# Kernel tuning notes

Measured on AMD Instinct MI355X. Metric: run time of the kernel, lower is better.

## Reference

```python
import jax, jax.numpy as jnp
import numpy as np

N_NODES = 50000
N_REL = 16
N_BASIS = 8
D_IN = 64
D_HID = 64
N_CLASS = 16
N_EDGES = 800000


def setup_inputs() -> dict:
    key = jax.random.key(0)
    ks = jax.random.split(key, 9)
    x = jax.random.normal(ks[0], (N_NODES, D_IN), dtype=jnp.float32)
    edge_index = jax.random.randint(ks[1], (2, N_EDGES), 0, N_NODES, dtype=jnp.int64)
    edge_type = jax.random.randint(ks[2], (N_EDGES,), 0, N_REL, dtype=jnp.int64)
    s1 = 1.0 / np.sqrt(D_IN)
    s2 = 1.0 / np.sqrt(D_HID)
    # layer 1: basis decomposition W_r = sum_b coeffs[r,b] * bases[b]
    bases1 = jax.random.normal(ks[3], (N_BASIS, D_IN, D_HID), dtype=jnp.float32) * s1
    coeffs1 = jax.random.normal(ks[4], (N_REL, N_BASIS), dtype=jnp.float32)
    self1 = jax.random.normal(ks[5], (D_IN, D_HID), dtype=jnp.float32) * s1
    # layer 2
    bases2 = jax.random.normal(ks[6], (N_BASIS, D_HID, N_CLASS), dtype=jnp.float32) * s2
    coeffs2 = jax.random.normal(ks[7], (N_REL, N_BASIS), dtype=jnp.float32)
    self2 = jax.random.normal(ks[8], (D_HID, N_CLASS), dtype=jnp.float32) * s2
    return {"x": x, "bases1": bases1, "coeffs1": coeffs1, "self1": self1,
            "bases2": bases2, "coeffs2": coeffs2, "self2": self2,
            "edge_index": edge_index, "edge_type": edge_type}


def _rgcn_layer(h, bases, coeffs, self_w, src, seg_id, inv_c):
    # normalized messages gathered from source nodes: [E, d]
    msg = h[src] * inv_c[:, None]
    # fused per-(relation, target-node) segment reduce -> [R, N, d]
    agg = jax.ops.segment_sum(msg, seg_id, num_segments=N_REL * N_NODES)
    agg = agg.reshape(N_REL, N_NODES, -1)
    # per-relation weights from basis decomposition: [R, d_in, d_out]
    w_rel = jnp.einsum('rb,bio->rio', coeffs, bases)
    return jnp.einsum('rni,rio->no', agg, w_rel) + h @ self_w


def reference(x, bases1, coeffs1, self1, bases2, coeffs2, self2, edge_index, edge_type):
    src, dst = edge_index[0], edge_index[1]
    # normalization constants: per-relation in-degree of each target node
    counts = jnp.zeros((N_REL, N_NODES), dtype=jnp.float32).at[edge_type, dst].add(1.0)
    inv_c = 1.0 / jnp.maximum(counts[edge_type, dst], 1.0)  # [E]
    seg_id = edge_type * N_NODES + dst  # combined (relation, node) segment key
    h = jax.nn.relu(_rgcn_layer(x, bases1, coeffs1, self1, src, seg_id, inv_c))
    logits = _rgcn_layer(h, bases2, coeffs2, self2, src, seg_id, inv_c)
    return logits
```

## Files before the change

kernel.cpp:

```cpp
#include <hip/hip_runtime.h>

#define N_NODES 50000
#define N_REL 16
#define N_BASIS 8
#define N_EDGES 800000
#define G1_BLOCKS 782
#define SC_BLOCKS 3125
#define WREL_BLOCKS 340
#define ZERO_BLOCKS 49
#define CAP 64

typedef short s8v __attribute__((ext_vector_type(8)));
typedef float f4v __attribute__((ext_vector_type(4)));

__device__ inline unsigned short f2bf(float f) {
    union { float f; unsigned u; } v; v.f = f;
    unsigned r = (v.u + 0x7FFFu + ((v.u >> 16) & 1u)) >> 16;
    return (unsigned short)r;
}
__device__ inline float bf2f(unsigned short b) {
    union { unsigned u; float f; } v; v.u = ((unsigned)b) << 16;
    return v.f;
}
__device__ __forceinline__ void acc8(float* a, float inv, int4 p) {
    a[0] += inv * __int_as_float((int)((unsigned)p.x << 16));
    a[1] += inv * __int_as_float(p.x & (int)0xFFFF0000u);
    a[2] += inv * __int_as_float((int)((unsigned)p.y << 16));
    a[3] += inv * __int_as_float(p.y & (int)0xFFFF0000u);
    a[4] += inv * __int_as_float((int)((unsigned)p.z << 16));
    a[5] += inv * __int_as_float(p.z & (int)0xFFFF0000u);
    a[6] += inv * __int_as_float((int)((unsigned)p.w << 16));
    a[7] += inv * __int_as_float(p.w & (int)0xFFFF0000u);
}

__global__ __launch_bounds__(256) void k_pre(const float* __restrict__ b1, const float* __restrict__ c1,
                                             const float* __restrict__ s1f,
                                             const float* __restrict__ b2, const float* __restrict__ c2,
                                             const float* __restrict__ s2f,
                                             unsigned short* __restrict__ w1T,
                                             unsigned short* __restrict__ w2T,
                                             int* __restrict__ cursor) {
    int bid = blockIdx.x;
    if (bid >= WREL_BLOCKS) {
        int i = (bid - WREL_BLOCKS) * 256 + threadIdx.x;
        if (i < 12504) ((int4*)cursor)[i] = make_int4(0, 0, 0, 0);
        return;
    }
    int idx = bid * 256 + threadIdx.x;
    if (idx < 17 * 4096) {
        int r = idx >> 12, o = (idx >> 6) & 63, k = idx & 63;
        float acc = 0.f;
        if (r < 16) {
            #pragma unroll
            for (int b = 0; b < N_BASIS; b++) acc += c1[r * N_BASIS + b] * b1[b * 4096 + k * 64 + o];
        } else {
            acc = s1f[k * 64 + o];
        }
        w1T[idx] = f2bf(acc);
    } else {
        int idx2 = idx - 17 * 4096;
        if (idx2 < 17 * 1024) {
            int r = idx2 >> 10, o = (idx2 >> 6) & 15, k = idx2 & 63;
            float acc = 0.f;
            if (r < 16) {
                #pragma unroll
                for (int b = 0; b < N_BASIS; b++) acc += c2[r * N_BASIS + b] * b2[b * 1024 + k * 16 + o];
            } else {
                acc = s2f[k * 16 + o];
            }
            w2T[idx2] = f2bf(acc);
        }
    }
}

__device__ __forceinline__ void gemm1_tile(int tile, int tid,
                                           const float* __restrict__ x,
                                           const unsigned short* __restrict__ w1T,
                                           unsigned short* __restrict__ t1,
                                           unsigned short* __restrict__ h,
                                           unsigned short* wbuf,
                                           unsigned short* ou) {
    int wv = tid >> 6, lane = tid & 63;
    int m = lane & 15, q = lane >> 4;
    int nb = tile * 64 + wv * 16;
    bool active = (nb < N_NODES);
    int n = active ? (nb + m) : 0;

    const float* xr = x + (size_t)n * 64 + q * 8;
    float4 x0a = *(const float4*)(xr);
    float4 x0b = *(const float4*)(xr + 4);
    float4 x1a = *(const float4*)(xr + 32);
    float4 x1b = *(const float4*)(xr + 36);
    s8v b0, b1;
    b0[0] = f2bf(x0a.x); b0[1] = f2bf(x0a.y); b0[2] = f2bf(x0a.z); b0[3] = f2bf(x0a.w);
    b0[4] = f2bf(x0b.x); b0[5] = f2bf(x0b.y); b0[6] = f2bf(x0b.z); b0[7] = f2bf(x0b.w);
    b1[0] = f2bf(x1a.x); b1[1] = f2bf(x1a.y); b1[2] = f2bf(x1a.z); b1[3] = f2bf(x1a.w);
    b1[4] = f2bf(x1b.x); b1[5] = f2bf(x1b.y); b1[6] = f2bf(x1b.z); b1[7] = f2bf(x1b.w);

    int c0 = tid, c1 = tid + 256;
    int p0s = (c0 >> 3) * 64 + (((c0 & 7) ^ ((c0 >> 3) & 7)) << 3);
    int p1s = (c1 >> 3) * 64 + (((c1 & 7) ^ ((c1 >> 3) & 7)) << 3);

    {
        const int4* src = (const int4*)w1T;
        int4 v0 = src[c0], v1 = src[c1];
        *(int4*)&wbuf[p0s] = v0;
        *(int4*)&wbuf[p1s] = v1;
    }
    __syncthreads();

    for (int w = 0; w < 17; w++) {
        int cur = w & 1;
        if (w < 16) {
            const int4* src = (const int4*)w1T + (w + 1) * 512;
            int4 v0 = src[c0], v1 = src[c1];
            *(int4*)&wbuf[(cur ^ 1) * 4096 + p0s] = v0;
            *(int4*)&wbuf[(cur ^ 1) * 4096 + p1s] = v1;
        }
        #pragma unroll
        for (int ct = 0; ct < 4; ct++) {
            int ro = ct * 16 + m;
            int pa = q ^ (ro & 7);
            int pb = (4 + q) ^ (ro & 7);
            s8v A0 = *(const s8v*)&wbuf[cur * 4096 + ro * 64 + pa * 8];
            s8v A1 = *(const s8v*)&wbuf[cur * 4096 + ro * 64 + pb * 8];
            f4v acc = (f4v){0.f, 0.f, 0.f, 0.f};
            acc = __builtin_amdgcn_mfma_f32_16x16x32_bf16(A0, b0, acc, 0, 0, 0);
            acc = __builtin_amdgcn_mfma_f32_16x16x32_bf16(A1, b1, acc, 0, 0, 0);
            ushort4 o4;
            o4.x = f2bf(acc[0]); o4.y = f2bf(acc[1]); o4.z = f2bf(acc[2]); o4.w = f2bf(acc[3]);
            int g = ct * 2 + (q >> 1);
            int pg = g ^ (m & 7);
            *(ushort4*)&ou[wv * 1024 + m * 64 + pg * 8 + (q & 1) * 4] = o4;
        }
        if (active) {
            int r1 = lane >> 3, g1 = lane & 7;
            int pg1 = g1 ^ (r1 & 7);
            int4 d0 = *(const int4*)&ou[wv * 1024 + r1 * 64 + pg1 * 8];
            int4 d1 = *(const int4*)&ou[wv * 1024 + (r1 + 8) * 64 + pg1 * 8];
            unsigned short* base = (w < 16) ? (t1 + ((size_t)w * N_NODES + nb) * 64)
                                            : (h + (size_t)nb * 64);
            *(int4*)(base + lane * 8) = d0;
            *(int4*)(base + 512 + lane * 8) = d1;
        }
        __syncthreads();
    }
}

__global__ __launch_bounds__(256) void k_fused1(const float* __restrict__ x,
                                                const unsigned short* __restrict__ w1T,
                                                unsigned short* __restrict__ t1,
                                                unsigned short* __restrict__ h,
                                                const int* __restrict__ ei,
                                                const int* __restrict__ et,
                                                int* __restrict__ cursor,
                                                int* __restrict__ sed) {
    __shared__ __align__(16) unsigned short wbuf[2 * 4096];
    __shared__ __align__(16) unsigned short ou[4 * 1024];
    if (blockIdx.x >= G1_BLOCKS) {
        int e = (blockIdx.x - G1_BLOCKS) * 256 + threadIdx.x;
        if (e < N_EDGES) {
            int src = ei[e];
            int dst = ei[N_EDGES + e];
            int t = et[e];
            int pos = atomicAdd(&cursor[dst], 1);
            if (pos < CAP) sed[dst * CAP + pos] = (t << 16) | src;
        }
        return;
    }
    gemm1_tile(blockIdx.x, threadIdx.x, x, w1T, t1, h, wbuf, ou);
}

__global__ __launch_bounds__(256) void k_agg1(const int* __restrict__ cursor,
                                              const int* __restrict__ sed,
                                              const unsigned short* __restrict__ t1,
                                              unsigned short* __restrict__ h) {
    __shared__ int hist[4][16];
    int tid = threadIdx.x;
    int wv = tid >> 6, lane = tid & 63;
    int n = blockIdx.x * 4 + wv;
    int deg = cursor[n];
    deg = deg < CAP ? deg : CAP;
    const int* bucket = sed + n * CAP;

    if (lane < 16) hist[wv][lane] = 0;
    __syncthreads();
    if (lane < deg) {
        int en = bucket[lane];
        atomicAdd(&hist[wv][en >> 16], 1);
    }
    __syncthreads();

    int slot = lane >> 3;
    int d8 = lane & 7;
    float a[8];
    #pragma unroll
    for (int j = 0; j < 8; j++) a[j] = 0.f;
    for (int i = slot; i < deg; i += 16) {
        int e0 = bucket[i];
        bool has1 = (i + 8) < deg;
        int e1 = has1 ? bucket[i + 8] : e0;
        int t0 = e0 >> 16, s0 = e0 & 0xFFFF;
        int t1i = e1 >> 16, s1 = e1 & 0xFFFF;
        float inv0 = 1.0f / (float)hist[wv][t0];
        float inv1 = has1 ? (1.0f / (float)hist[wv][t1i]) : 0.f;
        int4 p0 = *(const int4*)(t1 + ((size_t)(t0 * N_NODES + s0)) * 64 + d8 * 8);
        int4 p1 = *(const int4*)(t1 + ((size_t)(t1i * N_NODES + s1)) * 64 + d8 * 8);
        acc8(a, inv0, p0);
        acc8(a, inv1, p1);
    }
    #pragma unroll
    for (int j = 0; j < 8; j++) {
        a[j] += __shfl_xor(a[j], 8, 64);
        a[j] += __shfl_xor(a[j], 16, 64);
        a[j] += __shfl_xor(a[j], 32, 64);
    }
    if (slot == 0) {
        size_t hi = (size_t)n * 64 + d8 * 8;
        int4 hv = *(const int4*)(h + hi);
        float b[8];
        b[0] = __int_as_float((int)((unsigned)hv.x << 16));
        b[1] = __int_as_float(hv.x & (int)0xFFFF0000u);
        b[2] = __int_as_float((int)((unsigned)hv.y << 16));
        b[3] = __int_as_float(hv.y & (int)0xFFFF0000u);
        b[4] = __int_as_float((int)((unsigned)hv.z << 16));
        b[5] = __int_as_float(hv.z & (int)0xFFFF0000u);
        b[6] = __int_as_float((int)((unsigned)hv.w << 16));
        b[7] = __int_as_float(hv.w & (int)0xFFFF0000u);
        ushort4 o0, o1;
        o0.x = f2bf(b[0] + a[0]); o0.y = f2bf(b[1] + a[1]);
        o0.z = f2bf(b[2] + a[2]); o0.w = f2bf(b[3] + a[3]);
        o1.x = f2bf(b[4] + a[4]); o1.y = f2bf(b[5] + a[5]);
        o1.z = f2bf(b[6] + a[6]); o1.w = f2bf(b[7] + a[7]);
        *(ushort4*)(h + hi) = o0;
        *(ushort4*)(h + hi + 4) = o1;
    }
}

__global__ __launch_bounds__(256) void k_gemm2(const unsigned short* __restrict__ h,
                                               const unsigned short* __restrict__ w2T,
                                               unsigned short* __restrict__ t2, float* __restrict__ out) {
    __shared__ __align__(16) unsigned short wall[272 * 64];
    int tid = threadIdx.x;
    int wv = tid >> 6, lane = tid & 63;
    int m = lane & 15, q = lane >> 4;
    int nb = blockIdx.x * 64 + wv * 16;

    for (int c = tid; c < 2176; c += 256) {
        int4 v = ((const int4*)w2T)[c];
        int row = c >> 3, g = c & 7;
        *(int4*)&wall[row * 64 + ((g ^ (row & 7)) << 3)] = v;
    }
    __syncthreads();
    if (nb >= N_NODES) return;
    int n = nb + m;

    s8v b0 = *(const s8v*)(h + (size_t)n * 64 + q * 8);
    s8v b1 = *(const s8v*)(h + (size_t)n * 64 + 32 + q * 8);
    #pragma unroll
    for (int j = 0; j < 8; j++) {
        if ((unsigned short)b0[j] & 0x8000u) b0[j] = 0;
        if ((unsigned short)b1[j] & 0x8000u) b1[j] = 0;
    }

    for (int w = 0; w < 17; w++) {
        int ro = w * 16 + m;
        int pa = q ^ (ro & 7);
        int pb = (4 + q) ^ (ro & 7);
        s8v A0 = *(const s8v*)&wall[ro * 64 + pa * 8];
        s8v A1 = *(const s8v*)&wall[ro * 64 + pb * 8];
        f4v acc = (f4v){0.f, 0.f, 0.f, 0.f};
        acc = __builtin_amdgcn_mfma_f32_16x16x32_bf16(A0, b0, acc, 0, 0, 0);
        acc = __builtin_amdgcn_mfma_f32_16x16x32_bf16(A1, b1, acc, 0, 0, 0);
        if (w < 16) {
            ushort4 o;
            o.x = f2bf(acc[0]); o.y = f2bf(acc[1]); o.z = f2bf(acc[2]); o.w = f2bf(acc[3]);
            *(ushort4*)(t2 + ((size_t)w * N_NODES + n) * 16 + q * 4) = o;
        } else {
            *(float4*)(out + (size_t)n * 16 + q * 4) = make_float4(acc[0], acc[1], acc[2], acc[3]);
        }
    }
}

__global__ __launch_bounds__(256) void k_agg2(const int* __restrict__ cursor,
                                              const int* __restrict__ sed,
                                              const unsigned short* __restrict__ t2,
                                              float* __restrict__ out) {
    __shared__ int hist[16][16];
    int tid = threadIdx.x;
    int j = tid >> 4;
    int sub = tid & 15;
    int n = blockIdx.x * 16 + j;
    int deg = cursor[n];
    deg = deg < CAP ? deg : CAP;
    const int* bucket = sed + n * CAP;

    hist[j][sub] = 0;
    __syncthreads();
    for (int i = sub; i < deg; i += 16) {
        int en = bucket[i];
        atomicAdd(&hist[j][en >> 16], 1);
    }
    __syncthreads();

    int slot = sub >> 1;
    int d2 = sub & 1;
    float a[8];
    #pragma unroll
    for (int k = 0; k < 8; k++) a[k] = 0.f;
    for (int i = slot; i < deg; i += 16) {
        int e0 = bucket[i];
        bool has1 = (i + 8) < deg;
        int e1 = has1 ? bucket[i + 8] : e0;
        int t0 = e0 >> 16, s0 = e0 & 0xFFFF;
        int t1i = e1 >> 16, s1 = e1 & 0xFFFF;
        float inv0 = 1.0f / (float)hist[j][t0];
        float inv1 = has1 ? (1.0f / (float)hist[j][t1i]) : 0.f;
        int4 p0 = *(const int4*)(t2 + ((size_t)(t0 * N_NODES + s0)) * 16 + d2 * 8);
        int4 p1 = *(const int4*)(t2 + ((size_t)(t1i * N_NODES + s1)) * 16 + d2 * 8);
        acc8(a, inv0, p0);
        acc8(a, inv1, p1);
    }
    #pragma unroll
    for (int k = 0; k < 8; k++) {
        a[k] += __shfl_xor(a[k], 2, 64);
        a[k] += __shfl_xor(a[k], 4, 64);
        a[k] += __shfl_xor(a[k], 8, 64);
    }
    if (slot == 0) {
        float* p = out + (size_t)n * 16 + d2 * 8;
        float4 c0 = *(const float4*)p;
        float4 c1 = *(const float4*)(p + 4);
        c0.x += a[0]; c0.y += a[1]; c0.z += a[2]; c0.w += a[3];
        c1.x += a[4]; c1.y += a[5]; c1.z += a[6]; c1.w += a[7];
        *(float4*)p = c0;
        *(float4*)(p + 4) = c1;
    }
}

extern "C" void kernel_launch(void* const* d_in, const int* in_sizes, int n_in,
                              void* d_out, int out_size, void* d_ws, size_t ws_size,
                              hipStream_t stream) {
    const float* x      = (const float*)d_in[0];
    const float* bases1 = (const float*)d_in[1];
    const float* coeffs1= (const float*)d_in[2];
    const float* self1  = (const float*)d_in[3];
    const float* bases2 = (const float*)d_in[4];
    const float* coeffs2= (const float*)d_in[5];
    const float* self2  = (const float*)d_in[6];
    const int*   ei     = (const int*)d_in[7];
    const int*   et     = (const int*)d_in[8];
    float* out = (float*)d_out;

    char* ws = (char*)d_ws;
    int*            cursor = (int*)(ws + 0);
    unsigned short* w1T    = (unsigned short*)(ws + 200064);
    unsigned short* w2T    = (unsigned short*)(ws + 339328);
    int*            sed    = (int*)(ws + 374144);
    unsigned short* h      = (unsigned short*)(ws + 13174144);
    unsigned short* t1     = (unsigned short*)(ws + 19574144);
    unsigned short* t2     = (unsigned short*)(ws + 121974144);

    k_pre<<<WREL_BLOCKS + ZERO_BLOCKS, 256, 0, stream>>>(
        bases1, coeffs1, self1, bases2, coeffs2, self2, w1T, w2T, cursor);
    k_fused1<<<G1_BLOCKS + SC_BLOCKS, 256, 0, stream>>>(x, w1T, t1, h, ei, et, cursor, sed);
    k_agg1<<<12500, 256, 0, stream>>>(cursor, sed, t1, h);
    k_gemm2<<<G1_BLOCKS, 256, 0, stream>>>(h, w2T, t2, out);
    k_agg2<<<SC_BLOCKS, 256, 0, stream>>>(cursor, sed, t2, out);
}
```

Before: 187.5 us.

## Partition edge bucketing into 8 sub-buckets to cut atomic contention

Edge scatter now splits each destination's cursor and bucket into 8 partitions chosen by block index (capacity 16 each), so concurrent atomics on the same node counter are spread out. The aggregation kernels first gather the partitions into a per-wave shared-memory list and then read edges from LDS. agg2 is remapped to one wave per node, with 4 lanes per 16-wide row and 16 edge slots per wave. The cost is an 8x larger cursor array to zero, more scattered bucket reads, and a risk of dropping edges if any partition sees more than 16 edges for one node.

```diff
diff --git a/kernel.cpp b/kernel.cpp
--- a/kernel.cpp
+++ b/kernel.cpp
@@ -7,8 +7,9 @@
 #define G1_BLOCKS 782
 #define SC_BLOCKS 3125
 #define WREL_BLOCKS 340
-#define ZERO_BLOCKS 49
-#define CAP 64
+#define ZERO_BLOCKS 391
+#define NPART 8
+#define CAPP 16
 
 typedef short s8v __attribute__((ext_vector_type(8)));
 typedef float f4v __attribute__((ext_vector_type(4)));
@@ -43,7 +44,7 @@
     int bid = blockIdx.x;
     if (bid >= WREL_BLOCKS) {
         int i = (bid - WREL_BLOCKS) * 256 + threadIdx.x;
-        if (i < 12504) ((int4*)cursor)[i] = make_int4(0, 0, 0, 0);
+        if (i < 100000) ((int4*)cursor)[i] = make_int4(0, 0, 0, 0);
         return;
     }
     int idx = bid * 256 + threadIdx.x;
@@ -159,37 +160,57 @@
     __shared__ __align__(16) unsigned short ou[4 * 1024];
     if (blockIdx.x >= G1_BLOCKS) {
         int e = (blockIdx.x - G1_BLOCKS) * 256 + threadIdx.x;
+        int p = blockIdx.x & 7;
         if (e < N_EDGES) {
             int src = ei[e];
             int dst = ei[N_EDGES + e];
             int t = et[e];
-            int pos = atomicAdd(&cursor[dst], 1);
-            if (pos < CAP) sed[dst * CAP + pos] = (t << 16) | src;
+            int pos = atomicAdd(&cursor[p * N_NODES + dst], 1);
+            if (pos < CAPP) sed[p * (N_NODES * CAPP) + dst * CAPP + pos] = (t << 16) | src;
         }
         return;
     }
     gemm1_tile(blockIdx.x, threadIdx.x, x, w1T, t1, h, wbuf, ou);
+}
+
+__device__ __forceinline__ int stage_node(int n, int lane,
+                                          const int* __restrict__ cursor,
+                                          const int* __restrict__ sed,
+                                          int* ent) {
+    int dp = 0;
+    if (lane < NPART) {
+        dp = cursor[lane * N_NODES + n];
+        dp = dp < CAPP ? dp : CAPP;
+    }
+    int p = lane >> 3, j = lane & 7;
+    int off = 0, deg = 0, mydeg = 0;
+    #pragma unroll
+    for (int q = 0; q < NPART; q++) {
+        int dq = __shfl(dp, q, 64);
+        if (q < p) off += dq;
+        if (q == p) mydeg = dq;
+        deg += dq;
+    }
+    const int* bucket = sed + p * (N_NODES * CAPP) + n * CAPP;
+    if (j < mydeg) ent[off + j] = bucket[j];
+    if (j + 8 < mydeg) ent[off + j + 8] = bucket[j + 8];
+    return deg;
 }
 
 __global__ __launch_bounds__(256) void k_agg1(const int* __restrict__ cursor,
                                               const int* __restrict__ sed,
                                               const unsigned short* __restrict__ t1,
                                               unsigned short* __restrict__ h) {
+    __shared__ int ent[4][128];
     __shared__ int hist[4][16];
     int tid = threadIdx.x;
     int wv = tid >> 6, lane = tid & 63;
     int n = blockIdx.x * 4 + wv;
-    int deg = cursor[n];
-    deg = deg < CAP ? deg : CAP;
-    const int* bucket = sed + n * CAP;
 
     if (lane < 16) hist[wv][lane] = 0;
-    __syncthreads();
-    if (lane < deg) {
-        int en = bucket[lane];
-        atomicAdd(&hist[wv][en >> 16], 1);
-    }
-    __syncthreads();
+    int deg = stage_node(n, lane, cursor, sed, ent[wv]);
+    if (lane < deg) atomicAdd(&hist[wv][ent[wv][lane] >> 16], 1);
+    if (lane + 64 < deg) atomicAdd(&hist[wv][ent[wv][lane + 64] >> 16], 1);
 
     int slot = lane >> 3;
     int d8 = lane & 7;
@@ -197,9 +218,9 @@
     #pragma unroll
     for (int j = 0; j < 8; j++) a[j] = 0.f;
     for (int i = slot; i < deg; i += 16) {
-        int e0 = bucket[i];
+        int e0 = ent[wv][i];
         bool has1 = (i + 8) < deg;
-        int e1 = has1 ? bucket[i + 8] : e0;
+        int e1 = has1 ? ent[wv][i + 8] : e0;
         int t0 = e0 >> 16, s0 = e0 & 0xFFFF;
         int t1i = e1 >> 16, s1 = e1 & 0xFFFF;
         float inv0 = 1.0f / (float)hist[wv][t0];
@@ -286,55 +307,47 @@
                                               const int* __restrict__ sed,
                                               const unsigned short* __restrict__ t2,
                                               float* __restrict__ out) {
-    __shared__ int hist[16][16];
+    __shared__ int ent[4][128];
+    __shared__ int hist[4][16];
     int tid = threadIdx.x;
-    int j = tid >> 4;
-    int sub = tid & 15;
-    int n = blockIdx.x * 16 + j;
-    int deg = cursor[n];
-    deg = deg < CAP ? deg : CAP;
-    const int* bucket = sed + n * CAP;
-
-    hist[j][sub] = 0;
-    __syncthreads();
-    for (int i = sub; i < deg; i += 16) {
-        int en = bucket[i];
-        atomicAdd(&hist[j][en >> 16], 1);
-    }
-    __syncthreads();
-
-    int slot = sub >> 1;
-    int d2 = sub & 1;
-    float a[8];
-    #pragma unroll
-    for (int k = 0; k < 8; k++) a[k] = 0.f;
-    for (int i = slot; i < deg; i += 16) {
-        int e0 = bucket[i];
-        bool has1 = (i + 8) < deg;
-        int e1 = has1 ? bucket[i + 8] : e0;
+    int wv = tid >> 6, lane = tid & 63;
+    int n = blockIdx.x * 4 + wv;
+
+    if (lane < 16) hist[wv][lane] = 0;
+    int deg = stage_node(n, lane, cursor, sed, ent[wv]);
+    if (lane < deg) atomicAdd(&hist[wv][ent[wv][lane] >> 16], 1);
+    if (lane + 64 < deg) atomicAdd(&hist[wv][ent[wv][lane + 64] >> 16], 1);
+
+    int slot = lane >> 2;
+    int d4 = lane & 3;
+    float a[4] = {0.f, 0.f, 0.f, 0.f};
+    for (int i = slot; i < deg; i += 32) {
+        int e0 = ent[wv][i];
+        bool has1 = (i + 16) < deg;
+        int e1 = has1 ? ent[wv][i + 16] : e0;
         int t0 = e0 >> 16, s0 = e0 & 0xFFFF;
         int t1i = e1 >> 16, s1 = e1 & 0xFFFF;
-        float inv0 = 1.0f / (float)hist[j][t0];
-        float inv1 = has1 ? (1.0f / (float)hist[j][t1i]) : 0.f;
-        int4 p0 = *(const int4*)(t2 + ((size_t)(t0 * N_NODES + s0)) * 16 + d2 * 8);
-        int4 p1 = *(const int4*)(t2 + ((size_t)(t1i * N_NODES + s1)) * 16 + d2 * 8);
-        acc8(a, inv0, p0);
-        acc8(a, inv1, p1);
-    }
-    #pragma unroll
-    for (int k = 0; k < 8; k++) {
-        a[k] += __shfl_xor(a[k], 2, 64);
+        float inv0 = 1.0f / (float)hist[wv][t0];
+        float inv1 = has1 ? (1.0f / (float)hist[wv][t1i]) : 0.f;
+        ushort4 v0 = *(const ushort4*)(t2 + ((size_t)(t0 * N_NODES + s0)) * 16 + d4 * 4);
+        ushort4 v1 = *(const ushort4*)(t2 + ((size_t)(t1i * N_NODES + s1)) * 16 + d4 * 4);
+        a[0] += inv0 * bf2f(v0.x) + inv1 * bf2f(v1.x);
+        a[1] += inv0 * bf2f(v0.y) + inv1 * bf2f(v1.y);
+        a[2] += inv0 * bf2f(v0.z) + inv1 * bf2f(v1.z);
+        a[3] += inv0 * bf2f(v0.w) + inv1 * bf2f(v1.w);
+    }
+    #pragma unroll
+    for (int k = 0; k < 4; k++) {
         a[k] += __shfl_xor(a[k], 4, 64);
         a[k] += __shfl_xor(a[k], 8, 64);
+        a[k] += __shfl_xor(a[k], 16, 64);
+        a[k] += __shfl_xor(a[k], 32, 64);
     }
     if (slot == 0) {
-        float* p = out + (size_t)n * 16 + d2 * 8;
-        float4 c0 = *(const float4*)p;
-        float4 c1 = *(const float4*)(p + 4);
-        c0.x += a[0]; c0.y += a[1]; c0.z += a[2]; c0.w += a[3];
-        c1.x += a[4]; c1.y += a[5]; c1.z += a[6]; c1.w += a[7];
-        *(float4*)p = c0;
-        *(float4*)(p + 4) = c1;
+        float* p = out + (size_t)n * 16 + d4 * 4;
+        float4 c = *(const float4*)p;
+        c.x += a[0]; c.y += a[1]; c.z += a[2]; c.w += a[3];
+        *(float4*)p = c;
     }
 }
 
@@ -354,17 +367,17 @@
 
     char* ws = (char*)d_ws;
     int*            cursor = (int*)(ws + 0);
-    unsigned short* w1T    = (unsigned short*)(ws + 200064);
-    unsigned short* w2T    = (unsigned short*)(ws + 339328);
-    int*            sed    = (int*)(ws + 374144);
-    unsigned short* h      = (unsigned short*)(ws + 13174144);
-    unsigned short* t1     = (unsigned short*)(ws + 19574144);
-    unsigned short* t2     = (unsigned short*)(ws + 121974144);
+    unsigned short* w1T    = (unsigned short*)(ws + 1600000);
+    unsigned short* w2T    = (unsigned short*)(ws + 1739264);
+    int*            sed    = (int*)(ws + 1774080);
+    unsigned short* h      = (unsigned short*)(ws + 27374080);
+    unsigned short* t1     = (unsigned short*)(ws + 33774080);
+    unsigned short* t2     = (unsigned short*)(ws + 136174080);
 
     k_pre<<<WREL_BLOCKS + ZERO_BLOCKS, 256, 0, stream>>>(
         bases1, coeffs1, self1, bases2, coeffs2, self2, w1T, w2T, cursor);
     k_fused1<<<G1_BLOCKS + SC_BLOCKS, 256, 0, stream>>>(x, w1T, t1, h, ei, et, cursor, sed);
     k_agg1<<<12500, 256, 0, stream>>>(cursor, sed, t1, h);
     k_gemm2<<<G1_BLOCKS, 256, 0, stream>>>(h, w2T, t2, out);
-    k_agg2<<<SC_BLOCKS, 256, 0, stream>>>(cursor, sed, t2, out);
-}
+    k_agg2<<<12500, 256, 0, stream>>>(cursor, sed, t2, out);
+}
```

Result: slower. 192.0 us (+2.4%).

## Fuse layer-1 aggregation with layer-2 transform GEMM and drop histogram barriers

Applied to the files above, without the earlier changes.

Merges the layer-1 neighbour aggregation and the layer-2 per-relation MFMA transform into one kernel. Each block aggregates 16 nodes, applies ReLU, stages the rows in LDS and multiplies them by w2T read straight from global memory. This removes a kernel launch and the bf16 write and re-read of the hidden activations. Aggregation now uses 16 threads per node instead of a full wave, and the __syncthreads around the per-node LDS degree histograms are removed in both aggregation kernels. That removal relies on each 16-thread group sitting inside one wavefront.

```diff
diff --git a/kernel.cpp b/kernel.cpp
--- a/kernel.cpp
+++ b/kernel.cpp
@@ -171,114 +171,91 @@
     gemm1_tile(blockIdx.x, threadIdx.x, x, w1T, t1, h, wbuf, ou);
 }
 
-__global__ __launch_bounds__(256) void k_agg1(const int* __restrict__ cursor,
+__global__ __launch_bounds__(256) void k_aggt(const int* __restrict__ cursor,
                                               const int* __restrict__ sed,
                                               const unsigned short* __restrict__ t1,
-                                              unsigned short* __restrict__ h) {
-    __shared__ int hist[4][16];
+                                              const unsigned short* __restrict__ h,
+                                              const unsigned short* __restrict__ w2T,
+                                              unsigned short* __restrict__ t2,
+                                              float* __restrict__ out) {
+    __shared__ int hist[16][16];
+    __shared__ __align__(16) unsigned short htile[16][72];
     int tid = threadIdx.x;
-    int wv = tid >> 6, lane = tid & 63;
-    int n = blockIdx.x * 4 + wv;
+    int nb = blockIdx.x * 16;
+    int j = tid >> 4;
+    int sub = tid & 15;
+    int n = nb + j;
     int deg = cursor[n];
     deg = deg < CAP ? deg : CAP;
     const int* bucket = sed + n * CAP;
 
-    if (lane < 16) hist[wv][lane] = 0;
-    __syncthreads();
-    if (lane < deg) {
-        int en = bucket[lane];
-        atomicAdd(&hist[wv][en >> 16], 1);
-    }
-    __syncthreads();
-
-    int slot = lane >> 3;
-    int d8 = lane & 7;
+    hist[j][sub] = 0;
+    for (int i = sub; i < deg; i += 16)
+        atomicAdd(&hist[j][bucket[i] >> 16], 1);
+
+    int slot = sub >> 3;
+    int d8 = sub & 7;
     float a[8];
     #pragma unroll
-    for (int j = 0; j < 8; j++) a[j] = 0.f;
-    for (int i = slot; i < deg; i += 16) {
+    for (int k = 0; k < 8; k++) a[k] = 0.f;
+    for (int i = slot; i < deg; i += 4) {
         int e0 = bucket[i];
-        bool has1 = (i + 8) < deg;
-        int e1 = has1 ? bucket[i + 8] : e0;
+        bool has1 = (i + 2) < deg;
+        int e1 = has1 ? bucket[i + 2] : e0;
         int t0 = e0 >> 16, s0 = e0 & 0xFFFF;
         int t1i = e1 >> 16, s1 = e1 & 0xFFFF;
-        float inv0 = 1.0f / (float)hist[wv][t0];
-        float inv1 = has1 ? (1.0f / (float)hist[wv][t1i]) : 0.f;
+        float inv0 = 1.0f / (float)hist[j][t0];
+        float inv1 = has1 ? (1.0f / (float)hist[j][t1i]) : 0.f;
         int4 p0 = *(const int4*)(t1 + ((size_t)(t0 * N_NODES + s0)) * 64 + d8 * 8);
         int4 p1 = *(const int4*)(t1 + ((size_t)(t1i * N_NODES + s1)) * 64 + d8 * 8);
         acc8(a, inv0, p0);
         acc8(a, inv1, p1);
     }
     #pragma unroll
-    for (int j = 0; j < 8; j++) {
-        a[j] += __shfl_xor(a[j], 8, 64);
-        a[j] += __shfl_xor(a[j], 16, 64);
-        a[j] += __shfl_xor(a[j], 32, 64);
-    }
+    for (int k = 0; k < 8; k++) a[k] += __shfl_xor(a[k], 8, 64);
     if (slot == 0) {
-        size_t hi = (size_t)n * 64 + d8 * 8;
-        int4 hv = *(const int4*)(h + hi);
-        float b[8];
-        b[0] = __int_as_float((int)((unsigned)hv.x << 16));
-        b[1] = __int_as_float(hv.x & (int)0xFFFF0000u);
-        b[2] = __int_as_float((int)((unsigned)hv.y << 16));
-        b[3] = __int_as_float(hv.y & (int)0xFFFF0000u);
-        b[4] = __int_as_float((int)((unsigned)hv.z << 16));
-        b[5] = __int_as_float(hv.z & (int)0xFFFF0000u);
-        b[6] = __int_as_float((int)((unsigned)hv.w << 16));
-        b[7] = __int_as_float(hv.w & (int)0xFFFF0000u);
-        ushort4 o0, o1;
-        o0.x = f2bf(b[0] + a[0]); o0.y = f2bf(b[1] + a[1]);
-        o0.z = f2bf(b[2] + a[2]); o0.w = f2bf(b[3] + a[3]);
-        o1.x = f2bf(b[4] + a[4]); o1.y = f2bf(b[5] + a[5]);
-        o1.z = f2bf(b[6] + a[6]); o1.w = f2bf(b[7] + a[7]);
-        *(ushort4*)(h + hi) = o0;
-        *(ushort4*)(h + hi + 4) = o1;
-    }
-}
-
-__global__ __launch_bounds__(256) void k_gemm2(const unsigned short* __restrict__ h,
-                                               const unsigned short* __restrict__ w2T,
-                                               unsigned short* __restrict__ t2, float* __restrict__ out) {
-    __shared__ __align__(16) unsigned short wall[272 * 64];
-    int tid = threadIdx.x;
+        int4 hs = *(const int4*)(h + (size_t)n * 64 + d8 * 8);
+        acc8(a, 1.0f, hs);
+        ushort4 lo, hi;
+        lo.x = f2bf(a[0] > 0.f ? a[0] : 0.f);
+        lo.y = f2bf(a[1] > 0.f ? a[1] : 0.f);
+        lo.z = f2bf(a[2] > 0.f ? a[2] : 0.f);
+        lo.w = f2bf(a[3] > 0.f ? a[3] : 0.f);
+        hi.x = f2bf(a[4] > 0.f ? a[4] : 0.f);
+        hi.y = f2bf(a[5] > 0.f ? a[5] : 0.f);
+        hi.z = f2bf(a[6] > 0.f ? a[6] : 0.f);
+        hi.w = f2bf(a[7] > 0.f ? a[7] : 0.f);
+        *(ushort4*)&htile[j][d8 * 8] = lo;
+        *(ushort4*)&htile[j][d8 * 8 + 4] = hi;
+    }
+    __syncthreads();
+
     int wv = tid >> 6, lane = tid & 63;
     int m = lane & 15, q = lane >> 4;
-    int nb = blockIdx.x * 64 + wv * 16;
-
-    for (int c = tid; c < 2176; c += 256) {
-        int4 v = ((const int4*)w2T)[c];
-        int row = c >> 3, g = c & 7;
-        *(int4*)&wall[row * 64 + ((g ^ (row & 7)) << 3)] = v;
-    }
-    __syncthreads();
-    if (nb >= N_NODES) return;
-    int n = nb + m;
-
-    s8v b0 = *(const s8v*)(h + (size_t)n * 64 + q * 8);
-    s8v b1 = *(const s8v*)(h + (size_t)n * 64 + 32 + q * 8);
-    #pragma unroll
-    for (int j = 0; j < 8; j++) {
-        if ((unsigned short)b0[j] & 0x8000u) b0[j] = 0;
-        if ((unsigned short)b1[j] & 0x8000u) b1[j] = 0;
-    }
-
-    for (int w = 0; w < 17; w++) {
-        int ro = w * 16 + m;
-        int pa = q ^ (ro & 7);
-        int pb = (4 + q) ^ (ro & 7);
-        s8v A0 = *(const s8v*)&wall[ro * 64 + pa * 8];
-        s8v A1 = *(const s8v*)&wall[ro * 64 + pb * 8];
+    int nn = nb + m;
+    s8v b0 = *(const s8v*)&htile[m][q * 8];
+    s8v b1 = *(const s8v*)&htile[m][32 + q * 8];
+    const unsigned short* wp = w2T + m * 64 + q * 8;
+
+    #pragma unroll
+    for (int j5 = 0; j5 < 4; j5++) {
+        int w = wv * 4 + j5;
+        s8v A0 = *(const s8v*)(wp + (w << 10));
+        s8v A1 = *(const s8v*)(wp + (w << 10) + 32);
         f4v acc = (f4v){0.f, 0.f, 0.f, 0.f};
         acc = __builtin_amdgcn_mfma_f32_16x16x32_bf16(A0, b0, acc, 0, 0, 0);
         acc = __builtin_amdgcn_mfma_f32_16x16x32_bf16(A1, b1, acc, 0, 0, 0);
-        if (w < 16) {
-            ushort4 o;
-            o.x = f2bf(acc[0]); o.y = f2bf(acc[1]); o.z = f2bf(acc[2]); o.w = f2bf(acc[3]);
-            *(ushort4*)(t2 + ((size_t)w * N_NODES + n) * 16 + q * 4) = o;
-        } else {
-            *(float4*)(out + (size_t)n * 16 + q * 4) = make_float4(acc[0], acc[1], acc[2], acc[3]);
-        }
+        ushort4 o;
+        o.x = f2bf(acc[0]); o.y = f2bf(acc[1]); o.z = f2bf(acc[2]); o.w = f2bf(acc[3]);
+        *(ushort4*)(t2 + ((size_t)w * N_NODES + nn) * 16 + q * 4) = o;
+    }
+    if (wv == 0) {
+        s8v A0 = *(const s8v*)(wp + (16 << 10));
+        s8v A1 = *(const s8v*)(wp + (16 << 10) + 32);
+        f4v acc = (f4v){0.f, 0.f, 0.f, 0.f};
+        acc = __builtin_amdgcn_mfma_f32_16x16x32_bf16(A0, b0, acc, 0, 0, 0);
+        acc = __builtin_amdgcn_mfma_f32_16x16x32_bf16(A1, b1, acc, 0, 0, 0);
+        *(float4*)(out + (size_t)nn * 16 + q * 4) = make_float4(acc[0], acc[1], acc[2], acc[3]);
     }
 }
 
@@ -296,12 +273,8 @@
     const int* bucket = sed + n * CAP;
 
     hist[j][sub] = 0;
-    __syncthreads();
-    for (int i = sub; i < deg; i += 16) {
-        int en = bucket[i];
-        atomicAdd(&hist[j][en >> 16], 1);
-    }
-    __syncthreads();
+    for (int i = sub; i < deg; i += 16)
+        atomicAdd(&hist[j][bucket[i] >> 16], 1);
 
     int slot = sub >> 1;
     int d2 = sub & 1;
@@ -364,7 +337,6 @@
     k_pre<<<WREL_BLOCKS + ZERO_BLOCKS, 256, 0, stream>>>(
         bases1, coeffs1, self1, bases2, coeffs2, self2, w1T, w2T, cursor);
     k_fused1<<<G1_BLOCKS + SC_BLOCKS, 256, 0, stream>>>(x, w1T, t1, h, ei, et, cursor, sed);
-    k_agg1<<<12500, 256, 0, stream>>>(cursor, sed, t1, h);
-    k_gemm2<<<G1_BLOCKS, 256, 0, stream>>>(h, w2T, t2, out);
+    k_aggt<<<SC_BLOCKS, 256, 0, stream>>>(cursor, sed, t1, h, w2T, t2, out);
     k_agg2<<<SC_BLOCKS, 256, 0, stream>>>(cursor, sed, t2, out);
 }
```

New measurement: 181.9 us. 1.03x faster.
